# Kernel optimization log

Hardware: AMD Instinct MI355X
Metric: run time of the kernel (lower is better)

## Reference

```python
import jax, jax.numpy as jnp
import numpy as np

N = 100_000   # nodes per node type (A, B)
H = 128       # hidden_size == input feature dim
E = 600_000   # edges per relation
L = 2         # num_layers
R = 3         # relations: 0:(A->B), 1:(B->B), 2:(B->A)
AA = 64       # attn_size
C = 16        # num_classes
NEG_SLOPE = 0.01
BN_EPS = 1.0


def setup_inputs() -> dict:
    key = jax.random.key(0)
    ks = jax.random.split(key, 24)
    s = 1.0 / np.sqrt(H)
    inp = {
        "xA": jax.random.normal(ks[0], (N, H), jnp.float32),
        "xB": jax.random.normal(ks[1], (N, H), jnp.float32),
        "Wsrc": jax.random.uniform(ks[2], (L, R, H, H), jnp.float32, -s, s),
        "bsrc": jax.random.uniform(ks[3], (L, R, H), jnp.float32, -s, s),
        "Wdst": jax.random.uniform(ks[4], (L, R, H, H), jnp.float32, -s, s),
        "bdst": jax.random.uniform(ks[5], (L, R, H), jnp.float32, -s, s),
        "Wupd": jax.random.uniform(ks[6], (L, R, 2 * H, H), jnp.float32, -s, s),
        "bupd": jax.random.uniform(ks[7], (L, R, H), jnp.float32, -s, s),
        "attnW1": jax.random.uniform(ks[8], (L, H, AA), jnp.float32, -s, s),
        "attnb1": jax.random.uniform(ks[9], (L, AA), jnp.float32, -s, s),
        "attnw2": jax.random.uniform(ks[10], (L, AA), jnp.float32, -s, s),
        "gamma": jnp.ones((L, 2, H), jnp.float32),
        "beta": jnp.zeros((L, 2, H), jnp.float32),
        "fcW": jax.random.uniform(ks[11], (2, H, C), jnp.float32, -s, s),
        "fcb": jax.random.uniform(ks[12], (2, C), jnp.float32, -s, s),
        "eAB": jax.random.randint(ks[13], (2, E), 0, N, jnp.int32),
        "eBB": jax.random.randint(ks[14], (2, E), 0, N, jnp.int32),
        "eBA": jax.random.randint(ks[15], (2, E), 0, N, jnp.int32),
    }
    return inp


def _scatter_mean(src_feat, dst_idx, num_dst):
    # mean-aggregate gathered src features onto dst nodes (SpMM mean)
    seg = jax.ops.segment_sum(src_feat, dst_idx, num_segments=num_dst)
    cnt = jax.ops.segment_sum(
        jnp.ones((dst_idx.shape[0], 1), src_feat.dtype), dst_idx, num_segments=num_dst)
    return seg / jnp.maximum(cnt, 1.0)


def reference(xA, xB, Wsrc, bsrc, Wdst, bdst, Wupd, bupd,
              attnW1, attnb1, attnw2, gamma, beta, fcW, fcb,
              eAB, eBB, eBA):

    def conv(l, r, xs, xd, e):
        aggr = _scatter_mean(xs[e[0]], e[1], xd.shape[0])   # [Nd, H]
        h = jnp.concatenate(
            [xd @ Wdst[l, r] + bdst[l, r], aggr @ Wsrc[l, r] + bsrc[l, r]], axis=-1)
        return h @ Wupd[l, r] + bupd[l, r]

    def attn_combine(xs, l):
        # xs: [K, N, H]; per-relation attention score, softmax over K (detached)
        s = jnp.tanh(xs @ attnW1[l] + attnb1[l]) @ attnw2[l]   # [K, N]
        alpha = jax.lax.stop_gradient(jax.nn.softmax(s.mean(axis=-1)))  # [K]
        return jnp.einsum('k,knh->nh', alpha, xs)

    def bn(x, g, b):
        mu = x.mean(axis=0)
        var = x.var(axis=0)  # biased, as torch BN training forward
        return (x - mu) / jnp.sqrt(var + BN_EPS) * g + b

    def leaky(x):
        return jnp.where(x >= 0, x, NEG_SLOPE * x)

    for l in range(L):
        embB1 = conv(l, 0, xA, xB, eAB)  # A -> B
        embB2 = conv(l, 1, xB, xB, eBB)  # B -> B
        embA = conv(l, 2, xB, xA, eBA)   # B -> A (single relation, no combine)
        xB_new = attn_combine(jnp.stack([embB1, embB2]), l)
        xA = leaky(bn(embA, gamma[l, 0], beta[l, 0]))
        xB = leaky(bn(xB_new, gamma[l, 1], beta[l, 1]))

    outA = xA @ fcW[0] + fcb[0]
    outB = xB @ fcW[1] + fcb[1]
    return jnp.stack([outA, outB])  # [2, N, C]
```

## Files before the change

kernel.cpp:

```cpp
#include <hip/hip_runtime.h>

#define NN 100000
#define HH 128
#define EE 600000
#define LL 2
#define RR 3
#define AAA 64
#define CC 16
#define SCAN_B 98
#define ATTN_GRID ((NN + 127) / 128)

typedef unsigned short u16;
typedef unsigned int u32;
typedef __attribute__((ext_vector_type(8))) short bf16x8;
typedef __attribute__((ext_vector_type(4))) float f32x4;

__device__ inline u16 f2bf(float f) {
    unsigned int u = __float_as_uint(f);
    return (u16)((u + 0x7FFF + ((u >> 16) & 1)) >> 16);
}
__device__ inline float bf2f(u16 h) { return __uint_as_float((unsigned int)h << 16); }

__device__ __forceinline__ int hi_off(int gi, int r) { return (gi * 32) ^ ((r & 7) << 4); }
__device__ __forceinline__ int lo_off(int gi, int r) { return (gi * 32 + 16) ^ ((r & 7) << 4); }

__device__ __forceinline__ void stage16(const void* g, void* l) {
    __builtin_amdgcn_global_load_lds((const __attribute__((address_space(1))) unsigned int*)g,
                                     (__attribute__((address_space(3))) unsigned int*)l, 16, 0, 0);
}

__global__ void k_fuse_w(const float* __restrict__ Wsrc, const float* __restrict__ Wdst,
                         const float* __restrict__ Wupd, u16* __restrict__ Wdt_hi,
                         u16* __restrict__ Wdt_lo, u16* __restrict__ Wst_hi,
                         u16* __restrict__ Wst_lo) {
    int b = blockIdx.x;
    int lr = b >> 7, i = b & 127;
    int t = threadIdx.x;
    int j = t & 127;
    const float* wu = Wupd + (size_t)lr * 2 * HH * HH;
    float acc = 0.f;
    size_t o = ((size_t)lr * HH + j) * HH + i;
    if (t < 128) {
        const float* wd = Wdst + ((size_t)lr * HH + i) * HH;
        for (int k = 0; k < HH; ++k) acc += wd[k] * wu[k * HH + j];
        u16 h = f2bf(acc);
        Wdt_hi[o] = h;
        Wdt_lo[o] = f2bf(acc - bf2f(h));
    } else {
        const float* wsc = Wsrc + ((size_t)lr * HH + i) * HH;
        for (int k = 0; k < HH; ++k) acc += wsc[k] * wu[(HH + k) * HH + j];
        u16 h = f2bf(acc);
        Wst_hi[o] = h;
        Wst_lo[o] = f2bf(acc - bf2f(h));
    }
}

__global__ void k_fuse_b(const float* __restrict__ bsrc, const float* __restrict__ bdst,
                         const float* __restrict__ bupd, const float* __restrict__ Wupd,
                         float* __restrict__ fB) {
    int lr = blockIdx.x;
    int j = threadIdx.x;
    const float* wu = Wupd + (size_t)lr * 2 * HH * HH;
    const float* bd = bdst + lr * HH;
    const float* bs = bsrc + lr * HH;
    float acc = bupd[lr * HH + j];
    for (int k = 0; k < HH; ++k)
        acc += bd[k] * wu[k * HH + j] + bs[k] * wu[(HH + k) * HH + j];
    fB[lr * HH + j] = acc;
}

__global__ void k_fuse_a(const float* __restrict__ W1, u16* __restrict__ Ah,
                         u16* __restrict__ Al) {
    int b = blockIdx.x;
    int l = b >> 6, a = b & 63;
    int k = threadIdx.x;
    float v = W1[((size_t)l * HH + k) * AAA + a];
    u16 h = f2bf(v);
    size_t o = (size_t)b * HH + k;
    Ah[o] = h;
    Al[o] = f2bf(v - bf2f(h));
}

__global__ void k_count(const int* __restrict__ e0, const int* __restrict__ e1,
                        const int* __restrict__ e2, int* __restrict__ cnt,
                        int* __restrict__ pose) {
    int rel = blockIdx.y;
    const int* d = (rel == 0 ? e0 : rel == 1 ? e1 : e2) + EE;
    int i = blockIdx.x * 256 + threadIdx.x;
    if (i < EE) pose[rel * EE + i] = atomicAdd(&cnt[rel * NN + d[i]], 1);
}

__global__ void k_scan1(const int* __restrict__ cnt_all, int* __restrict__ rs_all,
                        int* __restrict__ bsum) {
    __shared__ int sd[256];
    int rel = blockIdx.y;
    const int* cnt = cnt_all + rel * NN;
    int* rs = rs_all + rel * NN;
    int blk = blockIdx.x, tid = threadIdx.x;
    int base = blk * 1024 + tid * 4;
    int c0 = 0, c1 = 0, c2 = 0, c3 = 0;
    if (base + 0 < NN) c0 = cnt[base + 0];
    if (base + 1 < NN) c1 = cnt[base + 1];
    if (base + 2 < NN) c2 = cnt[base + 2];
    if (base + 3 < NN) c3 = cnt[base + 3];
    int s = c0 + c1 + c2 + c3;
    sd[tid] = s;
    __syncthreads();
    for (int off = 1; off < 256; off <<= 1) {
        int v = (tid >= off) ? sd[tid - off] : 0;
        __syncthreads();
        sd[tid] += v;
        __syncthreads();
    }
    int excl = sd[tid] - s;
    if (tid == 255) bsum[rel * 128 + blk] = sd[255];
    if (base + 0 < NN) rs[base + 0] = excl;
    if (base + 1 < NN) rs[base + 1] = excl + c0;
    if (base + 2 < NN) rs[base + 2] = excl + c0 + c1;
    if (base + 3 < NN) rs[base + 3] = excl + c0 + c1 + c2;
}

__global__ void k_scan2(int* __restrict__ bsum) {
    __shared__ int sd[128];
    int rel = blockIdx.x;
    int tid = threadIdx.x;
    int v = (tid < SCAN_B) ? bsum[rel * 128 + tid] : 0;
    sd[tid] = v;
    __syncthreads();
    for (int off = 1; off < 128; off <<= 1) {
        int u = (tid >= off) ? sd[tid - off] : 0;
        __syncthreads();
        sd[tid] += u;
        __syncthreads();
    }
    if (tid < SCAN_B) bsum[rel * 128 + tid] = sd[tid] - v;
}

__global__ void k_scan3(int* __restrict__ rs_all, const int* __restrict__ bsum) {
    int rel = blockIdx.y;
    int i = blockIdx.x * 256 + threadIdx.x;
    if (i < NN) rs_all[rel * NN + i] += bsum[rel * 128 + (i >> 10)];
}

__global__ void k_fill(const int* __restrict__ e0, const int* __restrict__ e1,
                       const int* __restrict__ e2, const int* __restrict__ pose,
                       const int* __restrict__ rs_all, int* __restrict__ csr_all) {
    int rel = blockIdx.y;
    const int* e = rel == 0 ? e0 : rel == 1 ? e1 : e2;
    int i = blockIdx.x * 256 + threadIdx.x;
    if (i >= EE) return;
    int s = e[i], d = e[EE + i];
    csr_all[(size_t)rel * EE + rs_all[rel * NN + d] + pose[rel * EE + i]] = s;
}

__global__ __launch_bounds__(256) void k_aggr(u16* __restrict__ Xp, const float* __restrict__ xs,
                                              const int* __restrict__ rs, const int* __restrict__ cnt,
                                              const int* __restrict__ csr) {
    int node = blockIdx.x * 4 + (threadIdx.x >> 6);
    if (node >= NN) return;
    int lane = threadIdx.x & 63;
    int beg = rs[node], deg = cnt[node];
    const float2* xs2 = (const float2*)xs;
    float ax = 0.f, ay = 0.f;
    int j = 0;
    for (; j + 4 <= deg; j += 4) {
        int s0 = csr[beg + j], s1 = csr[beg + j + 1];
        int s2 = csr[beg + j + 2], s3 = csr[beg + j + 3];
        float2 v0 = xs2[(size_t)s0 * 64 + lane];
        float2 v1 = xs2[(size_t)s1 * 64 + lane];
        float2 v2 = xs2[(size_t)s2 * 64 + lane];
        float2 v3 = xs2[(size_t)s3 * 64 + lane];
        ax += (v0.x + v1.x) + (v2.x + v3.x);
        ay += (v0.y + v1.y) + (v2.y + v3.y);
    }
    if (j + 2 <= deg) {
        int s0 = csr[beg + j], s1 = csr[beg + j + 1];
        float2 v0 = xs2[(size_t)s0 * 64 + lane];
        float2 v1 = xs2[(size_t)s1 * 64 + lane];
        ax += v0.x + v1.x;
        ay += v0.y + v1.y;
        j += 2;
    }
    if (j < deg) {
        float2 v = xs2[(size_t)csr[beg + j] * 64 + lane];
        ax += v.x;
        ay += v.y;
    }
    float sc = 1.0f / fmaxf((float)deg, 1.0f);
    float vx = ax * sc, vy = ay * sc;
    u16 hx = f2bf(vx), hy = f2bf(vy);
    u16 lx = f2bf(vx - bf2f(hx)), ly = f2bf(vy - bf2f(hy));
    int g = lane >> 2;
    char* base = (char*)Xp + (size_t)node * 512 + (g >> 2) * 128;
    int jb = (lane & 3) * 4;
    __builtin_nontemporal_store(((u32)hy << 16) | hx, (u32*)(base + hi_off(g & 3, node) + jb));
    __builtin_nontemporal_store(((u32)ly << 16) | lx, (u32*)(base + lo_off(g & 3, node) + jb));
}

__global__ __launch_bounds__(256) void k_cgemm(float* Y, const u16* X1p,
                                               const float* __restrict__ X2,
                                               const u16* __restrict__ W1h, const u16* __restrict__ W1l,
                                               const u16* __restrict__ W2h, const u16* __restrict__ W2l,
                                               const float* __restrict__ bias, int nrows) {
    __shared__ __attribute__((aligned(16))) char Xt[16384];
    int tid = threadIdx.x;
    int row0 = blockIdx.x * 128;
    int lane = tid & 63, wv = tid >> 6;
    int l15 = lane & 15, lg = lane >> 4;
    bool full = (row0 + 128 <= nrows);

    f32x4 acc[8][2];
#pragma unroll
    for (int i = 0; i < 8; ++i)
#pragma unroll
        for (int j = 0; j < 2; ++j) acc[i][j] = (f32x4)(0.f);

    for (int ph = 0; ph < 2; ++ph) {
        const u16* Wh = ph ? W2h : W1h;
        const u16* Wl = ph ? W2l : W1l;
        for (int kc = 0; kc < HH; kc += 32) {
            __syncthreads();
            if (ph == 0) {
#pragma unroll
                for (int p = 0; p < 4; ++p) {
                    int tb = p * 4096 + tid * 16;
                    int r = tb >> 7, off = tb & 127;
                    stage16((const char*)X1p + (size_t)(row0 + r) * 512 + (kc >> 5) * 128 + off,
                            Xt + tb);
                }
            } else {
#pragma unroll
                for (int it = 0; it < 2; ++it) {
                    int g2 = tid + it * 256;
                    int r = g2 >> 2, gi = g2 & 3;
                    float4 a = make_float4(0.f, 0.f, 0.f, 0.f), b = a;
                    if (full || row0 + r < nrows) {
                        const float* xp = &X2[(size_t)(row0 + r) * HH + kc + gi * 8];
                        a = *(const float4*)xp;
                        b = *(const float4*)(xp + 4);
                    }
                    u16 h0 = f2bf(a.x), h1 = f2bf(a.y), h2 = f2bf(a.z), h3 = f2bf(a.w);
                    u16 h4 = f2bf(b.x), h5 = f2bf(b.y), h6 = f2bf(b.z), h7 = f2bf(b.w);
                    bf16x8 hv = {(short)h0, (short)h1, (short)h2, (short)h3,
                                 (short)h4, (short)h5, (short)h6, (short)h7};
                    bf16x8 lv = {(short)f2bf(a.x - bf2f(h0)), (short)f2bf(a.y - bf2f(h1)),
                                 (short)f2bf(a.z - bf2f(h2)), (short)f2bf(a.w - bf2f(h3)),
                                 (short)f2bf(b.x - bf2f(h4)), (short)f2bf(b.y - bf2f(h5)),
                                 (short)f2bf(b.z - bf2f(h6)), (short)f2bf(b.w - bf2f(h7))};
                    char* rb = Xt + r * 128;
                    *(bf16x8*)(rb + hi_off(gi, r)) = hv;
                    *(bf16x8*)(rb + lo_off(gi, r)) = lv;
                }
            }
            bf16x8 bh[2], bl[2];
#pragma unroll
            for (int nt = 0; nt < 2; ++nt) {
                int n = (wv * 2 + nt) * 16 + l15;
                bh[nt] = *(const bf16x8*)&Wh[(size_t)n * HH + kc + lg * 8];
                bl[nt] = *(const bf16x8*)&Wl[(size_t)n * HH + kc + lg * 8];
            }
            __syncthreads();
#pragma unroll
            for (int mt = 0; mt < 8; ++mt) {
                int r = mt * 16 + l15;
                const char* rb = Xt + r * 128;
                bf16x8 ah = *(const bf16x8*)(rb + hi_off(lg, r));
                bf16x8 al = *(const bf16x8*)(rb + lo_off(lg, r));
#pragma unroll
                for (int nt = 0; nt < 2; ++nt) {
                    acc[mt][nt] = __builtin_amdgcn_mfma_f32_16x16x32_bf16(ah, bh[nt], acc[mt][nt], 0, 0, 0);
                    acc[mt][nt] = __builtin_amdgcn_mfma_f32_16x16x32_bf16(ah, bl[nt], acc[mt][nt], 0, 0, 0);
                    acc[mt][nt] = __builtin_amdgcn_mfma_f32_16x16x32_bf16(al, bh[nt], acc[mt][nt], 0, 0, 0);
                }
            }
        }
    }
#pragma unroll
    for (int mt = 0; mt < 8; ++mt)
#pragma unroll
        for (int nt = 0; nt < 2; ++nt) {
            int ncol = (wv * 2 + nt) * 16 + l15;
            float bv = bias[ncol];
#pragma unroll
            for (int j = 0; j < 4; ++j) {
                int r = row0 + mt * 16 + lg * 4 + j;
                if (r < nrows) Y[(size_t)r * HH + ncol] = acc[mt][nt][j] + bv;
            }
        }
}

__global__ __launch_bounds__(256) void k_attn(const float* __restrict__ XA, const float* __restrict__ XB,
                                              const u16* __restrict__ Ah, const u16* __restrict__ Al,
                                              const float* __restrict__ b1, const float* __restrict__ w2,
                                              float* __restrict__ PA, float* __restrict__ PB, int nrows) {
    __shared__ __attribute__((aligned(16))) char Xt[16384];
    __shared__ float red[4];
    int tid = threadIdx.x;
    bool second = blockIdx.x >= ATTN_GRID;
    const float* X = second ? XB : XA;
    float* partial = second ? PB : PA;
    int row0 = (second ? blockIdx.x - ATTN_GRID : blockIdx.x) * 128;
    int lane = tid & 63, wv = tid >> 6;
    int l15 = lane & 15, lg = lane >> 4;
    bool full = (row0 + 128 <= nrows);

    f32x4 acc[8];
#pragma unroll
    for (int i = 0; i < 8; ++i) acc[i] = (f32x4)(0.f);

    for (int kc = 0; kc < HH; kc += 32) {
        __syncthreads();
#pragma unroll
        for (int it = 0; it < 2; ++it) {
            int g2 = tid + it * 256;
            int r = g2 >> 2, gi = g2 & 3;
            float4 a = make_float4(0.f, 0.f, 0.f, 0.f), b = a;
            if (full || row0 + r < nrows) {
                const float* xp = &X[(size_t)(row0 + r) * HH + kc + gi * 8];
                a = *(const float4*)xp;
                b = *(const float4*)(xp + 4);
            }
            u16 h0 = f2bf(a.x), h1 = f2bf(a.y), h2 = f2bf(a.z), h3 = f2bf(a.w);
            u16 h4 = f2bf(b.x), h5 = f2bf(b.y), h6 = f2bf(b.z), h7 = f2bf(b.w);
            bf16x8 hv = {(short)h0, (short)h1, (short)h2, (short)h3,
                         (short)h4, (short)h5, (short)h6, (short)h7};
            bf16x8 lv = {(short)f2bf(a.x - bf2f(h0)), (short)f2bf(a.y - bf2f(h1)),
                         (short)f2bf(a.z - bf2f(h2)), (short)f2bf(a.w - bf2f(h3)),
                         (short)f2bf(b.x - bf2f(h4)), (short)f2bf(b.y - bf2f(h5)),
                         (short)f2bf(b.z - bf2f(h6)), (short)f2bf(b.w - bf2f(h7))};
            char* rb = Xt + r * 128;
            *(bf16x8*)(rb + hi_off(gi, r)) = hv;
            *(bf16x8*)(rb + lo_off(gi, r)) = lv;
        }
        int a = wv * 16 + l15;
        bf16x8 bh = *(const bf16x8*)&Ah[(size_t)a * HH + kc + lg * 8];
        bf16x8 bl = *(const bf16x8*)&Al[(size_t)a * HH + kc + lg * 8];
        __syncthreads();
#pragma unroll
        for (int mt = 0; mt < 8; ++mt) {
            int r = mt * 16 + l15;
            const char* rb = Xt + r * 128;
            bf16x8 ah = *(const bf16x8*)(rb + hi_off(lg, r));
            bf16x8 al = *(const bf16x8*)(rb + lo_off(lg, r));
            acc[mt] = __builtin_amdgcn_mfma_f32_16x16x32_bf16(ah, bh, acc[mt], 0, 0, 0);
            acc[mt] = __builtin_amdgcn_mfma_f32_16x16x32_bf16(ah, bl, acc[mt], 0, 0, 0);
            acc[mt] = __builtin_amdgcn_mfma_f32_16x16x32_bf16(al, bh, acc[mt], 0, 0, 0);
        }
    }
    float b1v = b1[wv * 16 + l15];
    float w2v = w2[wv * 16 + l15];
    float tot = 0.f;
#pragma unroll
    for (int mt = 0; mt < 8; ++mt)
#pragma unroll
        for (int j = 0; j < 4; ++j) {
            int r = row0 + mt * 16 + lg * 4 + j;
            if (r < nrows) tot += tanhf(acc[mt][j] + b1v) * w2v;
        }
#pragma unroll
    for (int off = 32; off > 0; off >>= 1) tot += __shfl_xor(tot, off);
    if (lane == 0) red[wv] = tot;
    __syncthreads();
    if (tid == 0)
        partial[second ? (blockIdx.x - ATTN_GRID) : blockIdx.x] = red[0] + red[1] + red[2] + red[3];
}

__global__ void k_alpha(const float* __restrict__ P1, const float* __restrict__ P2,
                        float* __restrict__ alpha, int nparts, float invn) {
    __shared__ float s1[256], s2[256];
    int tid = threadIdx.x;
    float a = 0.f, b = 0.f;
    for (int i = tid; i < nparts; i += 256) { a += P1[i]; b += P2[i]; }
    s1[tid] = a; s2[tid] = b;
    __syncthreads();
    for (int off = 128; off > 0; off >>= 1) {
        if (tid < off) { s1[tid] += s1[tid + off]; s2[tid] += s2[tid + off]; }
        __syncthreads();
    }
    if (tid == 0) {
        float m1 = s1[0] * invn, m2 = s2[0] * invn;
        float mx = fmaxf(m1, m2);
        float e1 = expf(m1 - mx), e2 = expf(m2 - mx);
        float inv = 1.f / (e1 + e2);
        alpha[0] = e1 * inv; alpha[1] = e2 * inv;
    }
}

template <bool COMBINE>
__global__ __launch_bounds__(256) void k_comb(float* __restrict__ X, const float* __restrict__ Y,
                                              const float* __restrict__ alpha, float* __restrict__ colsum,
                                              float* __restrict__ colsq, int nrows) {
    int tid = threadIdx.x;
    int h = tid & 127, half = tid >> 7;
    float a0 = 1.f, a1 = 0.f;
    if (COMBINE) { a0 = alpha[0]; a1 = alpha[1]; }
    float s = 0.f, q = 0.f;
    for (int n = blockIdx.x * 2 + half; n < nrows; n += gridDim.x * 2) {
        size_t off = (size_t)n * HH + h;
        float v = X[off];
        if (COMBINE) { v = a0 * v + a1 * Y[off]; X[off] = v; }
        s += v; q += v * v;
    }
    __shared__ float ls[256], lq[256];
    ls[tid] = s; lq[tid] = q;
    __syncthreads();
    if (half == 0) {
        atomicAdd(&colsum[h], ls[tid] + ls[tid + 128]);
        atomicAdd(&colsq[h], lq[tid] + lq[tid + 128]);
    }
}

__global__ void k_bnp(const float* __restrict__ sum, const float* __restrict__ sq,
                      const float* __restrict__ gamma, const float* __restrict__ beta,
                      float* __restrict__ scale, float* __restrict__ shift, float invn) {
    int h = threadIdx.x;
    float mu = sum[h] * invn;
    float var = sq[h] * invn - mu * mu;
    float sc = gamma[h] * rsqrtf(var + 1.0f);
    scale[h] = sc;
    shift[h] = beta[h] - mu * sc;
}

__global__ void k_bna(float* __restrict__ X0, float* __restrict__ X1,
                      const float* __restrict__ sc0, const float* __restrict__ sc1) {
    float* X = blockIdx.y ? X1 : X0;
    const float* scp = blockIdx.y ? sc1 : sc0;
    int i = blockIdx.x * 256 + threadIdx.x;
    float4 v = ((float4*)X)[i];
    int h0 = (i & 31) * 4;
    float4 sc = *(const float4*)&scp[h0];
    float4 sf = *(const float4*)&scp[128 + h0];
    v.x = v.x * sc.x + sf.x; v.y = v.y * sc.y + sf.y;
    v.z = v.z * sc.z + sf.z; v.w = v.w * sc.w + sf.w;
    v.x = v.x >= 0.f ? v.x : 0.01f * v.x;
    v.y = v.y >= 0.f ? v.y : 0.01f * v.y;
    v.z = v.z >= 0.f ? v.z : 0.01f * v.z;
    v.w = v.w >= 0.f ? v.w : 0.01f * v.w;
    ((float4*)X)[i] = v;
}

__global__ __launch_bounds__(256) void k_fc(const float* __restrict__ X0, const float* __restrict__ X1,
                                            const float* __restrict__ sc0, const float* __restrict__ sc1,
                                            const float* __restrict__ Wall, const float* __restrict__ ball,
                                            float* __restrict__ out, int nrows) {
    __shared__ float Xl[64 * 132];
    __shared__ float Wl[HH * CC];
    __shared__ float bl[CC];
    __shared__ float scl[HH], sfl[HH];
    int which = blockIdx.y;
    const float* X = which ? X1 : X0;
    const float* scp = which ? sc1 : sc0;
    const float* W = Wall + which * HH * CC;
    float* o = out + (size_t)which * NN * CC;
    int tid = threadIdx.x;
    int row0 = blockIdx.x * 64;
    for (int i = tid * 4; i < HH * CC; i += 1024)
        *(float4*)&Wl[i] = *(const float4*)&W[i];
    if (tid < CC) bl[tid] = ball[which * CC + tid];
    if (tid < HH) { scl[tid] = scp[tid]; sfl[tid] = scp[128 + tid]; }
    __syncthreads();
    for (int idx = tid; idx < 2048; idx += 256) {
        int r = idx >> 5, cc = idx & 31;
        int n = row0 + r;
        float4 v = make_float4(0.f, 0.f, 0.f, 0.f);
        if (n < nrows) v = *(const float4*)&X[(size_t)n * HH + cc * 4];
        float4 sc = *(const float4*)&scl[cc * 4];
        float4 sf = *(const float4*)&sfl[cc * 4];
        v.x = v.x * sc.x + sf.x; v.y = v.y * sc.y + sf.y;
        v.z = v.z * sc.z + sf.z; v.w = v.w * sc.w + sf.w;
        v.x = v.x >= 0.f ? v.x : 0.01f * v.x;
        v.y = v.y >= 0.f ? v.y : 0.01f * v.y;
        v.z = v.z >= 0.f ? v.z : 0.01f * v.z;
        v.w = v.w >= 0.f ? v.w : 0.01f * v.w;
        *(float4*)&Xl[r * 132 + cc * 4] = v;
    }
    __syncthreads();
    int c = tid & 15, nl = tid >> 4;
    const float* x0 = &Xl[(nl + 0) * 132];
    const float* x1 = &Xl[(nl + 16) * 132];
    const float* x2 = &Xl[(nl + 32) * 132];
    const float* x3 = &Xl[(nl + 48) * 132];
    float a0 = bl[c], a1 = a0, a2 = a0, a3 = a0;
#pragma unroll 8
    for (int h = 0; h < HH; ++h) {
        float w = Wl[h * CC + c];
        a0 += x0[h] * w;
        a1 += x1[h] * w;
        a2 += x2[h] * w;
        a3 += x3[h] * w;
    }
    int n0 = row0 + nl;
    if (n0 < nrows) o[(size_t)n0 * CC + c] = a0;
    if (n0 + 16 < nrows) o[(size_t)(n0 + 16) * CC + c] = a1;
    if (n0 + 32 < nrows) o[(size_t)(n0 + 32) * CC + c] = a2;
    if (n0 + 48 < nrows) o[(size_t)(n0 + 48) * CC + c] = a3;
}

extern "C" void kernel_launch(void* const* d_in, const int* in_sizes, int n_in,
                              void* d_out, int out_size, void* d_ws, size_t ws_size,
                              hipStream_t stream) {
    const float* xA = (const float*)d_in[0];
    const float* xB = (const float*)d_in[1];
    const float* Wsrc = (const float*)d_in[2];
    const float* bsrc = (const float*)d_in[3];
    const float* Wdst = (const float*)d_in[4];
    const float* bdst = (const float*)d_in[5];
    const float* Wupd = (const float*)d_in[6];
    const float* bupd = (const float*)d_in[7];
    const float* attnW1 = (const float*)d_in[8];
    const float* attnb1 = (const float*)d_in[9];
    const float* attnw2 = (const float*)d_in[10];
    const float* gamma = (const float*)d_in[11];
    const float* beta = (const float*)d_in[12];
    const float* fcW = (const float*)d_in[13];
    const float* fcb = (const float*)d_in[14];
    const int* eAB = (const int*)d_in[15];
    const int* eBB = (const int*)d_in[16];
    const int* eBA = (const int*)d_in[17];
    float* out = (float*)d_out;

    float* ws = (float*)d_ws;
    const size_t NH = (size_t)NN * HH;
    const size_t LRHH = (size_t)LL * RR * HH * HH;
    const size_t LAH = (size_t)LL * AAA * HH;
    float* B0 = ws;
    float* B1 = B0 + NH;
    float* B2 = B1 + NH;
    float* B3 = B2 + NH;
    u16* uWdh = (u16*)(B3 + NH);
    u16* uWdl = uWdh + LRHH;
    u16* uWsh = uWdl + LRHH;
    u16* uWsl = uWsh + LRHH;
    u16* uA1h = uWsl + LRHH;
    u16* uA1l = uA1h + LAH;
    float* fB = (float*)(uA1l + LAH);
    float* csA = fB + LL * RR * HH;
    float* csB = csA + 256;
    float* scA = csB + 256;
    float* scB = scA + 256;
    float* P1 = scB + 256;
    float* P2 = P1 + 1024;
    float* alp = P2 + 1024;
    int* icnt = (int*)(alp + 64);
    int* irs = icnt + 3 * NN;
    int* icsr = irs + 3 * NN;
    int* ifill = icsr + 3 * EE;
    int* ibsum = ifill + 3 * NN;
    int* pose = (int*)B3;
    const float invN = 1.0f / (float)NN;

    k_fuse_w<<<LL * RR * HH, 256, 0, stream>>>(Wsrc, Wdst, Wupd, uWdh, uWdl, uWsh, uWsl);
    k_fuse_b<<<LL * RR, HH, 0, stream>>>(bsrc, bdst, bupd, Wupd, fB);
    k_fuse_a<<<LL * AAA, HH, 0, stream>>>(attnW1, uA1h, uA1l);

    hipMemsetAsync(icnt, 0, 3 * NN * 4, stream);
    k_count<<<dim3((EE + 255) / 256, 3), 256, 0, stream>>>(eAB, eBB, eBA, icnt, pose);
    k_scan1<<<dim3(SCAN_B, 3), 256, 0, stream>>>(icnt, irs, ibsum);
    k_scan2<<<3, 128, 0, stream>>>(ibsum);
    k_scan3<<<dim3((NN + 255) / 256, 3), 256, 0, stream>>>(irs, ibsum);
    k_fill<<<dim3((EE + 255) / 256, 3), 256, 0, stream>>>(eAB, eBB, eBA, pose, irs, icsr);

    const int GEMM_GRID = (NN + 127) / 128;
    const int AGGR_GRID = (NN + 3) / 4;

    auto conv = [&](float* dest, const float* xs, const float* xd, int rel, int lr) {
        k_aggr<<<AGGR_GRID, 256, 0, stream>>>((u16*)dest, xs, irs + rel * NN, icnt + rel * NN,
                                              icsr + (size_t)rel * EE);
        k_cgemm<<<GEMM_GRID, 256, 0, stream>>>(dest, (const u16*)dest, xd,
                                               uWsh + (size_t)lr * HH * HH, uWsl + (size_t)lr * HH * HH,
                                               uWdh + (size_t)lr * HH * HH, uWdl + (size_t)lr * HH * HH,
                                               fB + lr * HH, NN);
    };

    conv(B0, xA, xB, 0, 0);
    conv(B1, xB, xB, 1, 1);
    conv(B2, xB, xA, 2, 2);
    k_attn<<<2 * ATTN_GRID, 256, 0, stream>>>(B0, B1, uA1h, uA1l, attnb1, attnw2, P1, P2, NN);
    k_alpha<<<1, 256, 0, stream>>>(P1, P2, alp, ATTN_GRID, invN);
    hipMemsetAsync(csB, 0, 256 * 4, stream);
    k_comb<true><<<512, 256, 0, stream>>>(B0, B1, alp, csB, csB + 128, NN);
    hipMemsetAsync(csA, 0, 256 * 4, stream);
    k_comb<false><<<512, 256, 0, stream>>>(B2, nullptr, nullptr, csA, csA + 128, NN);
    k_bnp<<<1, 128, 0, stream>>>(csA, csA + 128, gamma + 0 * HH, beta + 0 * HH, scA, scA + 128, invN);
    k_bnp<<<1, 128, 0, stream>>>(csB, csB + 128, gamma + 1 * HH, beta + 1 * HH, scB, scB + 128, invN);
    k_bna<<<dim3((int)(NH / 4 / 256), 2), 256, 0, stream>>>(B2, B0, scA, scB);

    conv(B1, B2, B0, 0, 3);
    conv(B3, B0, B0, 1, 4);
    k_attn<<<2 * ATTN_GRID, 256, 0, stream>>>(B1, B3, uA1h + LAH / 2 * 0 + (size_t)1 * AAA * HH,
                                              uA1l + (size_t)1 * AAA * HH,
                                              attnb1 + AAA, attnw2 + AAA, P1, P2, NN);
    k_alpha<<<1, 256, 0, stream>>>(P1, P2, alp, ATTN_GRID, invN);
    hipMemsetAsync(csB, 0, 256 * 4, stream);
    k_comb<true><<<512, 256, 0, stream>>>(B1, B3, alp, csB, csB + 128, NN);
    conv(B3, B0, B2, 2, 5);
    hipMemsetAsync(csA, 0, 256 * 4, stream);
    k_comb<false><<<512, 256, 0, stream>>>(B3, nullptr, nullptr, csA, csA + 128, NN);
    k_bnp<<<1, 128, 0, stream>>>(csA, csA + 128, gamma + 2 * HH, beta + 2 * HH, scA, scA + 128, invN);
    k_bnp<<<1, 128, 0, stream>>>(csB, csB + 128, gamma + 3 * HH, beta + 3 * HH, scB, scB + 128, invN);

    k_fc<<<dim3((NN + 63) / 64, 2), 256, 0, stream>>>(B3, B1, scA, scB, fcW, fcb, out, NN);
}
```

Baseline: 1.093 ms.

## Fold BN+leaky into consumer loads and BN stats into GEMM epilogue

Removes the standalone BN-apply kernel by applying the scale/shift and leaky ReLU on the fly wherever the layer-2 aggregation and GEMM read the layer-1 outputs. It also drops the non-combining column-statistics pass by accumulating column sums and sums of squares in the GEMM epilogue with atomics. Separate scale buffers are added for layer 2 so the layer-1 values stay valid while their raw tensors are still being read. In exchange, the per-edge gathers now do extra FMA and select work, and atomics add some contention.

```diff
diff --git a/kernel.cpp b/kernel.cpp
--- a/kernel.cpp
+++ b/kernel.cpp
@@ -155,34 +155,50 @@
 
 __global__ __launch_bounds__(256) void k_aggr(u16* __restrict__ Xp, const float* __restrict__ xs,
                                               const int* __restrict__ rs, const int* __restrict__ cnt,
-                                              const int* __restrict__ csr) {
+                                              const int* __restrict__ csr,
+                                              const float* __restrict__ bnsc) {
     int node = blockIdx.x * 4 + (threadIdx.x >> 6);
     if (node >= NN) return;
     int lane = threadIdx.x & 63;
     int beg = rs[node], deg = cnt[node];
     const float2* xs2 = (const float2*)xs;
+    bool bn = bnsc != nullptr;
+    float2 scv = make_float2(1.f, 1.f), sfv = make_float2(0.f, 0.f);
+    if (bn) {
+        scv = ((const float2*)bnsc)[lane];
+        sfv = ((const float2*)(bnsc + 128))[lane];
+    }
+    auto xf = [&](float2 v) {
+        if (bn) {
+            v.x = v.x * scv.x + sfv.x;
+            v.y = v.y * scv.y + sfv.y;
+            v.x = v.x >= 0.f ? v.x : 0.01f * v.x;
+            v.y = v.y >= 0.f ? v.y : 0.01f * v.y;
+        }
+        return v;
+    };
     float ax = 0.f, ay = 0.f;
     int j = 0;
     for (; j + 4 <= deg; j += 4) {
         int s0 = csr[beg + j], s1 = csr[beg + j + 1];
         int s2 = csr[beg + j + 2], s3 = csr[beg + j + 3];
-        float2 v0 = xs2[(size_t)s0 * 64 + lane];
-        float2 v1 = xs2[(size_t)s1 * 64 + lane];
-        float2 v2 = xs2[(size_t)s2 * 64 + lane];
-        float2 v3 = xs2[(size_t)s3 * 64 + lane];
+        float2 v0 = xf(xs2[(size_t)s0 * 64 + lane]);
+        float2 v1 = xf(xs2[(size_t)s1 * 64 + lane]);
+        float2 v2 = xf(xs2[(size_t)s2 * 64 + lane]);
+        float2 v3 = xf(xs2[(size_t)s3 * 64 + lane]);
         ax += (v0.x + v1.x) + (v2.x + v3.x);
         ay += (v0.y + v1.y) + (v2.y + v3.y);
     }
     if (j + 2 <= deg) {
         int s0 = csr[beg + j], s1 = csr[beg + j + 1];
-        float2 v0 = xs2[(size_t)s0 * 64 + lane];
-        float2 v1 = xs2[(size_t)s1 * 64 + lane];
+        float2 v0 = xf(xs2[(size_t)s0 * 64 + lane]);
+        float2 v1 = xf(xs2[(size_t)s1 * 64 + lane]);
         ax += v0.x + v1.x;
         ay += v0.y + v1.y;
         j += 2;
     }
     if (j < deg) {
-        float2 v = xs2[(size_t)csr[beg + j] * 64 + lane];
+        float2 v = xf(xs2[(size_t)csr[beg + j] * 64 + lane]);
         ax += v.x;
         ay += v.y;
     }
@@ -201,7 +217,9 @@
                                                const float* __restrict__ X2,
                                                const u16* __restrict__ W1h, const u16* __restrict__ W1l,
                                                const u16* __restrict__ W2h, const u16* __restrict__ W2l,
-                                               const float* __restrict__ bias, int nrows) {
+                                               const float* __restrict__ bias, int nrows,
+                                               const float* __restrict__ bnsc2,
+                                               float* __restrict__ colsum) {
     __shared__ __attribute__((aligned(16))) char Xt[16384];
     int tid = threadIdx.x;
     int row0 = blockIdx.x * 128;
@@ -238,6 +256,24 @@
                         const float* xp = &X2[(size_t)(row0 + r) * HH + kc + gi * 8];
                         a = *(const float4*)xp;
                         b = *(const float4*)(xp + 4);
+                    }
+                    if (bnsc2) {
+                        const float* scp = bnsc2 + kc + gi * 8;
+                        const float* sfp = bnsc2 + 128 + kc + gi * 8;
+                        float4 s0 = *(const float4*)scp, s1 = *(const float4*)(scp + 4);
+                        float4 f0 = *(const float4*)sfp, f1 = *(const float4*)(sfp + 4);
+                        a.x = a.x * s0.x + f0.x; a.y = a.y * s0.y + f0.y;
+                        a.z = a.z * s0.z + f0.z; a.w = a.w * s0.w + f0.w;
+                        b.x = b.x * s1.x + f1.x; b.y = b.y * s1.y + f1.y;
+                        b.z = b.z * s1.z + f1.z; b.w = b.w * s1.w + f1.w;
+                        a.x = a.x >= 0.f ? a.x : 0.01f * a.x;
+                        a.y = a.y >= 0.f ? a.y : 0.01f * a.y;
+                        a.z = a.z >= 0.f ? a.z : 0.01f * a.z;
+                        a.w = a.w >= 0.f ? a.w : 0.01f * a.w;
+                        b.x = b.x >= 0.f ? b.x : 0.01f * b.x;
+                        b.y = b.y >= 0.f ? b.y : 0.01f * b.y;
+                        b.z = b.z >= 0.f ? b.z : 0.01f * b.z;
+                        b.w = b.w >= 0.f ? b.w : 0.01f * b.w;
                     }
                     u16 h0 = f2bf(a.x), h1 = f2bf(a.y), h2 = f2bf(a.z), h3 = f2bf(a.w);
                     u16 h4 = f2bf(b.x), h5 = f2bf(b.y), h6 = f2bf(b.z), h7 = f2bf(b.w);
@@ -276,17 +312,31 @@
         }
     }
 #pragma unroll
-    for (int mt = 0; mt < 8; ++mt)
-#pragma unroll
-        for (int nt = 0; nt < 2; ++nt) {
-            int ncol = (wv * 2 + nt) * 16 + l15;
-            float bv = bias[ncol];
+    for (int nt = 0; nt < 2; ++nt) {
+        int ncol = (wv * 2 + nt) * 16 + l15;
+        float bv = bias[ncol];
+        float s = 0.f, q = 0.f;
+#pragma unroll
+        for (int mt = 0; mt < 8; ++mt)
 #pragma unroll
             for (int j = 0; j < 4; ++j) {
                 int r = row0 + mt * 16 + lg * 4 + j;
-                if (r < nrows) Y[(size_t)r * HH + ncol] = acc[mt][nt][j] + bv;
+                if (r < nrows) {
+                    float y = acc[mt][nt][j] + bv;
+                    Y[(size_t)r * HH + ncol] = y;
+                    s += y;
+                    q += y * y;
+                }
+            }
+        if (colsum) {
+            s += __shfl_xor(s, 16); s += __shfl_xor(s, 32);
+            q += __shfl_xor(q, 16); q += __shfl_xor(q, 32);
+            if (lg == 0) {
+                atomicAdd(&colsum[ncol], s);
+                atomicAdd(&colsum[128 + ncol], q);
             }
         }
+    }
 }
 
 __global__ __launch_bounds__(256) void k_attn(const float* __restrict__ XA, const float* __restrict__ XB,
@@ -386,19 +436,17 @@
     }
 }
 
-template <bool COMBINE>
 __global__ __launch_bounds__(256) void k_comb(float* __restrict__ X, const float* __restrict__ Y,
                                               const float* __restrict__ alpha, float* __restrict__ colsum,
                                               float* __restrict__ colsq, int nrows) {
     int tid = threadIdx.x;
     int h = tid & 127, half = tid >> 7;
-    float a0 = 1.f, a1 = 0.f;
-    if (COMBINE) { a0 = alpha[0]; a1 = alpha[1]; }
+    float a0 = alpha[0], a1 = alpha[1];
     float s = 0.f, q = 0.f;
     for (int n = blockIdx.x * 2 + half; n < nrows; n += gridDim.x * 2) {
         size_t off = (size_t)n * HH + h;
-        float v = X[off];
-        if (COMBINE) { v = a0 * v + a1 * Y[off]; X[off] = v; }
+        float v = a0 * X[off] + a1 * Y[off];
+        X[off] = v;
         s += v; q += v * v;
     }
     __shared__ float ls[256], lq[256];
@@ -419,24 +467,6 @@
     float sc = gamma[h] * rsqrtf(var + 1.0f);
     scale[h] = sc;
     shift[h] = beta[h] - mu * sc;
-}
-
-__global__ void k_bna(float* __restrict__ X0, float* __restrict__ X1,
-                      const float* __restrict__ sc0, const float* __restrict__ sc1) {
-    float* X = blockIdx.y ? X1 : X0;
-    const float* scp = blockIdx.y ? sc1 : sc0;
-    int i = blockIdx.x * 256 + threadIdx.x;
-    float4 v = ((float4*)X)[i];
-    int h0 = (i & 31) * 4;
-    float4 sc = *(const float4*)&scp[h0];
-    float4 sf = *(const float4*)&scp[128 + h0];
-    v.x = v.x * sc.x + sf.x; v.y = v.y * sc.y + sf.y;
-    v.z = v.z * sc.z + sf.z; v.w = v.w * sc.w + sf.w;
-    v.x = v.x >= 0.f ? v.x : 0.01f * v.x;
-    v.y = v.y >= 0.f ? v.y : 0.01f * v.y;
-    v.z = v.z >= 0.f ? v.z : 0.01f * v.z;
-    v.w = v.w >= 0.f ? v.w : 0.01f * v.w;
-    ((float4*)X)[i] = v;
 }
 
 __global__ __launch_bounds__(256) void k_fc(const float* __restrict__ X0, const float* __restrict__ X1,
@@ -538,7 +568,9 @@
     float* csB = csA + 256;
     float* scA = csB + 256;
     float* scB = scA + 256;
-    float* P1 = scB + 256;
+    float* scA2 = scB + 256;
+    float* scB2 = scA2 + 256;
+    float* P1 = scB2 + 256;
     float* P2 = P1 + 1024;
     float* alp = P2 + 1024;
     int* icnt = (int*)(alp + 64);
@@ -563,41 +595,37 @@
     const int GEMM_GRID = (NN + 127) / 128;
     const int AGGR_GRID = (NN + 3) / 4;
 
-    auto conv = [&](float* dest, const float* xs, const float* xd, int rel, int lr) {
+    auto conv = [&](float* dest, const float* xs, const float* xd, int rel, int lr,
+                    const float* bn_xs, const float* bn_xd, float* stats) {
         k_aggr<<<AGGR_GRID, 256, 0, stream>>>((u16*)dest, xs, irs + rel * NN, icnt + rel * NN,
-                                              icsr + (size_t)rel * EE);
+                                              icsr + (size_t)rel * EE, bn_xs);
         k_cgemm<<<GEMM_GRID, 256, 0, stream>>>(dest, (const u16*)dest, xd,
                                                uWsh + (size_t)lr * HH * HH, uWsl + (size_t)lr * HH * HH,
                                                uWdh + (size_t)lr * HH * HH, uWdl + (size_t)lr * HH * HH,
-                                               fB + lr * HH, NN);
+                                               fB + lr * HH, NN, bn_xd, stats);
     };
 
-    conv(B0, xA, xB, 0, 0);
-    conv(B1, xB, xB, 1, 1);
-    conv(B2, xB, xA, 2, 2);
+    hipMemsetAsync(csA, 0, 512 * 4, stream);
+    conv(B0, xA, xB, 0, 0, nullptr, nullptr, nullptr);
+    conv(B1, xB, xB, 1, 1, nullptr, nullptr, nullptr);
+    conv(B2, xB, xA, 2, 2, nullptr, nullptr, csA);
     k_attn<<<2 * ATTN_GRID, 256, 0, stream>>>(B0, B1, uA1h, uA1l, attnb1, attnw2, P1, P2, NN);
     k_alpha<<<1, 256, 0, stream>>>(P1, P2, alp, ATTN_GRID, invN);
-    hipMemsetAsync(csB, 0, 256 * 4, stream);
-    k_comb<true><<<512, 256, 0, stream>>>(B0, B1, alp, csB, csB + 128, NN);
-    hipMemsetAsync(csA, 0, 256 * 4, stream);
-    k_comb<false><<<512, 256, 0, stream>>>(B2, nullptr, nullptr, csA, csA + 128, NN);
+    k_comb<<<512, 256, 0, stream>>>(B0, B1, alp, csB, csB + 128, NN);
     k_bnp<<<1, 128, 0, stream>>>(csA, csA + 128, gamma + 0 * HH, beta + 0 * HH, scA, scA + 128, invN);
     k_bnp<<<1, 128, 0, stream>>>(csB, csB + 128, gamma + 1 * HH, beta + 1 * HH, scB, scB + 128, invN);
-    k_bna<<<dim3((int)(NH / 4 / 256), 2), 256, 0, stream>>>(B2, B0, scA, scB);
-
-    conv(B1, B2, B0, 0, 3);
-    conv(B3, B0, B0, 1, 4);
-    k_attn<<<2 * ATTN_GRID, 256, 0, stream>>>(B1, B3, uA1h + LAH / 2 * 0 + (size_t)1 * AAA * HH,
-                                              uA1l + (size_t)1 * AAA * HH,
+
+    hipMemsetAsync(csA, 0, 512 * 4, stream);
+    conv(B1, B2, B0, 0, 3, scA, scB, nullptr);
+    conv(B3, B0, B0, 1, 4, scB, scB, nullptr);
+    k_attn<<<2 * ATTN_GRID, 256, 0, stream>>>(B1, B3, uA1h + (size_t)AAA * HH,
+                                              uA1l + (size_t)AAA * HH,
                                               attnb1 + AAA, attnw2 + AAA, P1, P2, NN);
     k_alpha<<<1, 256, 0, stream>>>(P1, P2, alp, ATTN_GRID, invN);
-    hipMemsetAsync(csB, 0, 256 * 4, stream);
-    k_comb<true><<<512, 256, 0, stream>>>(B1, B3, alp, csB, csB + 128, NN);
-    conv(B3, B0, B2, 2, 5);
-    hipMemsetAsync(csA, 0, 256 * 4, stream);
-    k_comb<false><<<512, 256, 0, stream>>>(B3, nullptr, nullptr, csA, csA + 128, NN);
-    k_bnp<<<1, 128, 0, stream>>>(csA, csA + 128, gamma + 2 * HH, beta + 2 * HH, scA, scA + 128, invN);
-    k_bnp<<<1, 128, 0, stream>>>(csB, csB + 128, gamma + 3 * HH, beta + 3 * HH, scB, scB + 128, invN);
-
-    k_fc<<<dim3((NN + 63) / 64, 2), 256, 0, stream>>>(B3, B1, scA, scB, fcW, fcb, out, NN);
-}
+    k_comb<<<512, 256, 0, stream>>>(B1, B3, alp, csB, csB + 128, NN);
+    conv(B3, B0, B2, 2, 5, scB, scA, csA);
+    k_bnp<<<1, 128, 0, stream>>>(csA, csA + 128, gamma + 2 * HH, beta + 2 * HH, scA2, scA2 + 128, invN);
+    k_bnp<<<1, 128, 0, stream>>>(csB, csB + 128, gamma + 3 * HH, beta + 3 * HH, scB2, scB2 + 128, invN);
+
+    k_fc<<<dim3((NN + 63) / 64, 2), 256, 0, stream>>>(B3, B1, scA2, scB2, fcW, fcb, out, NN);
+}
```

New measurement: 1.057 ms. 3.3% less time.
